# Performance work log

Hardware: AMD Instinct MI355X
Metric: run time of the kernel (lower is better)

## Reference

```python
import jax, jax.numpy as jnp
import numpy as np

B, J, D, H, W, AE, GH, NA, EH, L = 64, 20000, 32, 64, 4, 16, 24, 5000, 128, 32


def _ln(x, g=None, b=None, eps=1e-5):
    mu = x.mean(-1, keepdims=True)
    var = jnp.mean((x - mu) ** 2, axis=-1, keepdims=True)
    y = (x - mu) * jax.lax.rsqrt(var + eps)
    if g is not None:
        y = y * g + b
    return y


def setup_inputs():
    key = jax.random.key(0)
    ks = jax.random.split(key, 12)
    def rn(k, shape, s):
        return (jax.random.normal(k, shape) * s).astype(jnp.float32)
    return {
        "x": jax.random.normal(ks[0], (B, J), jnp.float32),
        "mask": jax.random.randint(ks[1], (B, J), 0, 2, jnp.int32),
        "atse_idx": jax.random.randint(ks[2], (J,), 0, NA, jnp.int32),
        "feature_embedding": jax.random.normal(ks[3], (J, D), jnp.float32),
        "atse_embedding": jax.random.normal(ks[4], (NA, AE), jnp.float32),
        "h_W1": rn(ks[5], (1 + D, H), 0.15), "h_b1": jnp.zeros((H,), jnp.float32),
        "h_ln1_g": jnp.ones((H,), jnp.float32), "h_ln1_b": jnp.zeros((H,), jnp.float32),
        "h_W2": rn(ks[6], (H, D), 0.12), "h_b2": jnp.zeros((D,), jnp.float32),
        "h_ln2_g": jnp.ones((D,), jnp.float32), "h_ln2_b": jnp.zeros((D,), jnp.float32),
        "g_W1": rn(ks[7], (D + AE, GH), 0.14), "g_b1": jnp.zeros((GH,), jnp.float32),
        "g_W2": rn(ks[8], (GH, W), 0.2), "g_b2": jnp.zeros((W,), jnp.float32),
        "c_W": rn(ks[9], (W * D, D), 0.09), "c_b": jnp.zeros((D,), jnp.float32),
        "c_ln_g": jnp.ones((D,), jnp.float32), "c_ln_b": jnp.zeros((D,), jnp.float32),
        "e_W1": rn(ks[10], (D, EH), 0.18), "e_b1": jnp.zeros((EH,), jnp.float32),
        "e_W2": rn(ks[11], (EH, 2 * L), 0.09), "e_b2": jnp.zeros((2 * L,), jnp.float32),
    }


def _forward(x, mask, atse_idx, feature_embedding, atse_embedding,
             h_W1, h_b1, h_ln1_g, h_ln1_b, h_W2, h_b2, h_ln2_g, h_ln2_b,
             g_W1, g_b1, g_W2, g_b2, c_W, c_b, c_ln_g, c_ln_b,
             e_W1, e_b1, e_W2, e_b2):
    TEMP = 1.0  # temperature_fixed=True -> scale = temperature_value
    Bv, Jv = x.shape
    Dv = feature_embedding.shape[1]
    # h-layer on all (b, j) pairs; LayerNorm/ReLU are per-row so this equals the
    # per-sample gather version on observed rows (unobserved rows get zero weight below).
    h_in = jnp.concatenate(
        [x[..., None], jnp.broadcast_to(feature_embedding[None], (Bv, Jv, Dv))], axis=-1)
    h = jax.nn.relu(_ln(h_in @ h_W1 + h_b1, h_ln1_g, h_ln1_b))
    h_out = jax.nn.relu(_ln(h @ h_W2 + h_b2, h_ln2_g, h_ln2_b))  # [B, J, D]
    # gate: [h_out | E_atse(j)] -> W head logits
    ae = atse_embedding[atse_idx]  # [J, AE]
    gate_in = jnp.concatenate(
        [h_out, jnp.broadcast_to(ae[None], (Bv, Jv, ae.shape[1]))], axis=-1)
    raw = jax.nn.relu(gate_in @ g_W1 + g_b1) @ g_W2 + g_b2  # [B, J, W]
    logits = jnp.clip(raw * TEMP, -10.0, 10.0)
    obs = mask.astype(bool)
    masked = jnp.where(obs[..., None], logits, -1e9)
    weights = jax.nn.softmax(masked, axis=1)  # softmax over observed junctions per head
    head_sums = jnp.einsum('bjw,bjd->bwd', weights, h_out)  # [B, W, D]
    Wn, Dn = head_sums.shape[1], head_sums.shape[2]
    combined = jax.nn.relu(_ln(head_sums.reshape(Bv, Wn * Dn) @ c_W + c_b, c_ln_g, c_ln_b))
    combined = jnp.where(obs.any(axis=1)[:, None], combined, 0.0)  # empty-mask rows -> zeros
    # encoder_mlp: scvi FCLayers, 2 layers, LayerNorm (no affine) + ReLU each
    e1 = jax.nn.relu(_ln(combined @ e_W1 + e_b1))
    mu_logvar = jax.nn.relu(_ln(e1 @ e_W2 + e_b2))
    mu, logvar = jnp.split(mu_logvar, 2, axis=-1)
    return mu, logvar


def reference(x, mask, atse_idx, feature_embedding, atse_embedding,
              h_W1, h_b1, h_ln1_g, h_ln1_b, h_W2, h_b2, h_ln2_g, h_ln2_b,
              g_W1, g_b1, g_W2, g_b2, c_W, c_b, c_ln_g, c_ln_b,
              e_W1, e_b1, e_W2, e_b2):
    return _forward(x, mask, atse_idx, feature_embedding, atse_embedding,
                    h_W1, h_b1, h_ln1_g, h_ln1_b, h_W2, h_b2, h_ln2_g, h_ln2_b,
                    g_W1, g_b1, g_W2, g_b2, c_W, c_b, c_ln_g, c_ln_b,
                    e_W1, e_b1, e_W2, e_b2)
```

## Files before the change

### kernel.cpp

```cpp
#include <hip/hip_runtime.h>
#include <hip/hip_bf16.h>
#include <math.h>

#define Bv 64
#define Jv 20000
#define NBT 8
#define NYB 125
#define ITERS 5

typedef __attribute__((ext_vector_type(8))) short short8;
typedef __attribute__((ext_vector_type(4))) float f32x4;
typedef __attribute__((ext_vector_type(2))) float f32x2;
typedef __attribute__((ext_vector_type(2))) unsigned int u32x2;

union U8 { short8 s; unsigned int u[4]; };

__device__ __forceinline__ unsigned short f2bf(float f) {
  unsigned int u = __float_as_uint(f);
  u += 0x7FFFu + ((u >> 16) & 1u);
  return (unsigned short)(u >> 16);
}
__device__ __forceinline__ unsigned int pkbf(float a, float b) {
  __hip_bfloat162 h = __float22bfloat162_rn(make_float2(a, b));
  union { __hip_bfloat162 h; unsigned int u; } c;
  c.h = h;
  return c.u;
}

__device__ __forceinline__ f32x2 pk_fma(f32x2 a, f32x2 b, f32x2 c) {
  return __builtin_elementwise_fma(a, b, c);
}
__device__ __forceinline__ f32x2 pk_max0(f32x2 a) {
  f32x2 z = {0.f, 0.f};
  return __builtin_elementwise_max(a, z);
}

template <int CTRL>
__device__ __forceinline__ float dppadd(float v) {
  int t = __builtin_amdgcn_update_dpp(0, __float_as_int(v), CTRL, 0xF, 0xF, true);
  return v + __int_as_float(t);
}
__device__ __forceinline__ float pl16sum(float v) {
  float a = v, b;
  asm("v_mov_b32 %1, %0\n\t"
      "v_permlane16_swap_b32 %0, %1"
      : "+v"(a), "=&v"(b));
  return a + b;
}
__device__ __forceinline__ float pl32sum(float v) {
  float a = v, b;
  asm("v_mov_b32 %1, %0\n\t"
      "v_permlane32_swap_b32 %0, %1"
      : "+v"(a), "=&v"(b));
  return a + b;
}

__global__ __launch_bounds__(256, 2) void pe_fused(
    const float* __restrict__ x, const int* __restrict__ mask,
    const int* __restrict__ atse_idx, const float* __restrict__ fe,
    const float* __restrict__ ae,
    const float* __restrict__ hW1, const float* __restrict__ hb1,
    const float* __restrict__ hl1g, const float* __restrict__ hl1b,
    const float* __restrict__ hW2, const float* __restrict__ hb2,
    const float* __restrict__ hl2g, const float* __restrict__ hl2b,
    const float* __restrict__ gW1, const float* __restrict__ gb1,
    const float* __restrict__ gW2, const float* __restrict__ gb2,
    float* __restrict__ acc_g, float* __restrict__ se_g) {
  __shared__ __align__(16) float s_pg[32 * 68];
  __shared__ __align__(16) float s_gb[32 * 24 + 16];
  __shared__ __align__(16) float s_pair[256 * 4];
  __shared__ __align__(16) float s_ae[32 * 20];
  __shared__ __align__(16) float s_w0[64], s_w0g[64], s_l1g[64], s_l1b[64];
  __shared__ __align__(16) float s_b2[32], s_l2g[32], s_l2b[32];
  __shared__ __align__(16) float s_gb1[24], s_gW2[96];
  __shared__ float s_gb2[4], s_scal[2];
  __shared__ __align__(16) float s_gW1aT[24 * 16];
  __shared__ unsigned char s_mk[256];
  __shared__ __align__(16) unsigned short s_ovl[256 * 36];

  int tid = threadIdx.x;
  int btile = blockIdx.x;
  int ytile = blockIdx.y;
  int lane = tid & 63, wv = tid >> 6;
  int li = lane & 15, quad = lane >> 4;
  unsigned short* s_h = s_ovl;
  unsigned short* s_gW1bf = (unsigned short*)s_pair;

  for (int i = tid; i < 768; i += 256) s_gW1bf[i] = f2bf(gW1[i]);
  for (int i = tid; i < 384; i += 256)
    s_gW1aT[i] = gW1[768 + (i & 15) * 24 + (i >> 4)];
  if (tid < 96) s_gW2[tid] = gW2[tid];
  if (tid < 64) { s_w0[tid] = hW1[tid]; s_l1g[tid] = hl1g[tid]; s_l1b[tid] = hl1b[tid]; }
  if (tid < 32) { s_b2[tid] = hb2[tid]; s_l2g[tid] = hl2g[tid]; s_l2b[tid] = hl2b[tid]; }
  if (tid < 24) s_gb1[tid] = gb1[tid];
  if (tid < 4) s_gb2[tid] = gb2[tid];
  if (tid >= 224 && tid < 240) s_gb[32 * 24 + (tid - 224)] = 0.f;

  short8 bW2[2][2];
#pragma unroll
  for (int kt = 0; kt < 2; ++kt)
#pragma unroll
    for (int nt = 0; nt < 2; ++nt) {
      U8 t;
#pragma unroll
      for (int p = 0; p < 4; ++p) {
        float lo = hW2[(kt * 32 + quad * 8 + 2 * p) * 32 + nt * 16 + li];
        float hi = hW2[(kt * 32 + quad * 8 + 2 * p + 1) * 32 + nt * 16 + li];
        t.u[p] = pkbf(lo, hi);
      }
      bW2[kt][nt] = t.s;
    }
  U8 bH;
#pragma unroll
  for (int p = 0; p < 4; ++p) {
    float lo = hW1[(1 + quad * 8 + 2 * p) * 64 + wv * 16 + li];
    float hi = hW1[(1 + quad * 8 + 2 * p + 1) * 64 + wv * 16 + li];
    bH.u[p] = pkbf(lo, hi);
  }
  float hb = hb1[wv * 16 + li];

  __syncthreads();
  if (tid < 64) s_w0g[tid] = s_w0[tid] * s_l1g[tid];
  if (tid == 64) {
    float sw = 0.f, qw = 0.f;
    for (int k = 0; k < 64; ++k) { float w = s_w0[k]; sw += w; qw = fmaf(w, w, qw); }
    s_scal[0] = sw; s_scal[1] = qw;
  }
  short8 aG0, aG1;
#pragma unroll
  for (int i = 0; i < 8; ++i) {
    int k = quad * 8 + i;
    aG0[i] = (short)s_gW1bf[k * 24 + li];
    aG1[i] = (li < 8) ? (short)s_gW1bf[k * 24 + 16 + li] : (short)0;
  }

  f32x4 racc[2][2];
#pragma unroll
  for (int a = 0; a < 2; ++a)
#pragma unroll
    for (int c = 0; c < 2; ++c) {
      racc[a][c][0] = 0.f; racc[a][c][1] = 0.f; racc[a][c][2] = 0.f; racc[a][c][3] = 0.f;
    }
  float seacc[2] = {0.f, 0.f};

  int jp8 = tid >> 3, b8 = tid & 7;
  int J0 = ytile * ITERS * 32;
  float xv; int mk;

  {
    if (tid < 128) {
      int jj = tid >> 2, q = tid & 3;
      int ai = atse_idx[J0 + jj];
      float4 av = *(const float4*)(ae + (size_t)ai * 16 + q * 4);
      *(float4*)(s_ae + jj * 20 + q * 4) = av;
    }
    size_t xo = (size_t)(btile * 8 + b8) * Jv + J0 + jp8;
    xv = x[xo];
    mk = mask[xo];
    f32x4 cP;
#pragma unroll
    for (int mt = 0; mt < 2; ++mt) {
      cP[0] = hb; cP[1] = hb; cP[2] = hb; cP[3] = hb;
      const float* fp = fe + (size_t)(J0 + mt * 16 + li) * 32 + quad * 8;
      float4 f0 = *(const float4*)fp;
      float4 f1 = *(const float4*)(fp + 4);
      U8 aF;
      aF.u[0] = pkbf(f0.x, f0.y); aF.u[1] = pkbf(f0.z, f0.w);
      aF.u[2] = pkbf(f1.x, f1.y); aF.u[3] = pkbf(f1.z, f1.w);
      cP = __builtin_amdgcn_mfma_f32_16x16x32_bf16(aF.s, bH.s, cP, 0, 0, 0);
#pragma unroll
      for (int r = 0; r < 4; ++r)
        s_pg[(mt * 16 + quad * 4 + r) * 68 + wv * 16 + li] = cP[r];
    }
  }
  __syncthreads();

  for (int it = 0; it < ITERS; ++it) {
    {
      int c0 = b8 * 3;
      const f32x2* ar2 = (const f32x2*)(s_ae + jp8 * 20);
      f32x2 A[8];
#pragma unroll
      for (int a = 0; a < 8; ++a) A[a] = ar2[a];
#pragma unroll
      for (int c = 0; c < 3; ++c) {
        const f32x2* tr2 = (const f32x2*)(s_gW1aT + (c0 + c) * 16);
        f32x2 g2 = {s_gb1[c0 + c], 0.f};
#pragma unroll
        for (int a = 0; a < 8; ++a) g2 = pk_fma(A[a], tr2[a], g2);
        s_gb[jp8 * 24 + c0 + c] = g2.x + g2.y;
      }
    }
    {
      const f32x2* pp2 = (const f32x2*)(s_pg + jp8 * 68 + b8 * 8);
      const f32x2* ww2 = (const f32x2*)(s_w0 + b8 * 8);
      f32x2 p2[4] = {pp2[0], pp2[1], pp2[2], pp2[3]};
      f32x2 s2 = (p2[0] + p2[1]) + (p2[2] + p2[3]);
      f32x2 q2 = pk_fma(p2[0], p2[0],
                 pk_fma(p2[1], p2[1],
                 pk_fma(p2[2], p2[2], p2[3] * p2[3])));
      f32x2 d2 = pk_fma(p2[0], ww2[0],
                 pk_fma(p2[1], ww2[1],
                 pk_fma(p2[2], ww2[2], p2[3] * ww2[3])));
      float sp = s2.x + s2.y, qp = q2.x + q2.y, dwp = d2.x + d2.y;
      sp = dppadd<0xB1>(sp); sp = dppadd<0x4E>(sp); sp = dppadd<0x141>(sp);
      qp = dppadd<0xB1>(qp); qp = dppadd<0x4E>(qp); qp = dppadd<0x141>(qp);
      dwp = dppadd<0xB1>(dwp); dwp = dppadd<0x4E>(dwp); dwp = dppadd<0x141>(dwp);
      if (b8 == 0) *(float4*)(s_pg + jp8 * 68 + 64) = make_float4(sp, qp, dwp, 0.f);
    }
    {
      float4 exv = *(const float4*)(s_pg + jp8 * 68 + 64);
      float mu1 = fmaf(xv, s_scal[0], exv.x) * 0.015625f;
      float Et2 = fmaf(xv * xv, s_scal[1], fmaf(2.0f * xv, exv.z, exv.y)) * 0.015625f;
      float rs1 = rsqrtf(fmaxf(Et2 - mu1 * mu1, 0.f) + 1e-5f);
      *(float4*)(s_pair + tid * 4) = make_float4(xv * rs1, rs1, -mu1 * rs1, 0.f);
      s_mk[tid] = (unsigned char)mk;
    }

    {
      f32x4 cd[4][2];
      float b2a = s_b2[li], b2b = s_b2[16 + li];
#pragma unroll
      for (int t = 0; t < 4; ++t) {
        cd[t][0][0] = b2a; cd[t][0][1] = b2a; cd[t][0][2] = b2a; cd[t][0][3] = b2a;
        cd[t][1][0] = b2b; cd[t][1][1] = b2b; cd[t][1][2] = b2b; cd[t][1][3] = b2b;
      }
#pragma unroll
      for (int kt = 0; kt < 2; ++kt) {
        int base = kt * 32 + quad * 8;
        float4 wg0 = *(const float4*)(s_w0g + base);
        float4 wg1 = *(const float4*)(s_w0g + base + 4);
        float4 gg0 = *(const float4*)(s_l1g + base);
        float4 gg1 = *(const float4*)(s_l1g + base + 4);
        float4 bb0 = *(const float4*)(s_l1b + base);
        float4 bb1 = *(const float4*)(s_l1b + base + 4);
        f32x2 wg2[4] = {{wg0.x, wg0.y}, {wg0.z, wg0.w}, {wg1.x, wg1.y}, {wg1.z, wg1.w}};
        f32x2 gg2[4] = {{gg0.x, gg0.y}, {gg0.z, gg0.w}, {gg1.x, gg1.y}, {gg1.z, gg1.w}};
        f32x2 bb2[4] = {{bb0.x, bb0.y}, {bb0.z, bb0.w}, {bb1.x, bb1.y}, {bb1.z, bb1.w}};
#pragma unroll
        for (int t = 0; t < 4; ++t) {
          int mrow = wv * 64 + t * 16 + li;
          float4 pr = *(const float4*)(s_pair + mrow * 4);
          f32x2 prx = {pr.x, pr.x}, pry = {pr.y, pr.y}, prz = {pr.z, pr.z};
          const float* pgp = s_pg + (mrow >> 3) * 68 + base;
          float4 p0 = *(const float4*)pgp;
          float4 p1 = *(const float4*)(pgp + 4);
          f32x2 pv2[4] = {{p0.x, p0.y}, {p0.z, p0.w}, {p1.x, p1.y}, {p1.z, p1.w}};
          U8 a8;
#pragma unroll
          for (int i = 0; i < 4; ++i) {
            f32x2 av2 = pk_max0(pk_fma(pk_fma(pry, pv2[i], prz), gg2[i],
                                       pk_fma(prx, wg2[i], bb2[i])));
            a8.u[i] = pkbf(av2.x, av2.y);
          }
          cd[t][0] = __builtin_amdgcn_mfma_f32_16x16x32_bf16(a8.s, bW2[kt][0], cd[t][0], 0, 0, 0);
          cd[t][1] = __builtin_amdgcn_mfma_f32_16x16x32_bf16(a8.s, bW2[kt][1], cd[t][1], 0, 0, 0);
        }
      }
      float g0 = s_l2g[li], be0 = s_l2b[li];
      float g1v = s_l2g[16 + li], be1 = s_l2b[16 + li];
#pragma unroll
      for (int t = 0; t < 4; ++t) {
        float sum[4], sq[4];
#pragma unroll
        for (int r = 0; r < 4; ++r) {
          float a = cd[t][0][r], b = cd[t][1][r];
          sum[r] = a + b;
          sq[r] = fmaf(a, a, b * b);
        }
#pragma unroll
        for (int r = 0; r < 4; ++r) {
          sum[r] = dppadd<0xB1>(sum[r]); sum[r] = dppadd<0x4E>(sum[r]);
          sum[r] = dppadd<0x124>(sum[r]); sum[r] = dppadd<0x128>(sum[r]);
          sq[r] = dppadd<0xB1>(sq[r]); sq[r] = dppadd<0x4E>(sq[r]);
          sq[r] = dppadd<0x124>(sq[r]); sq[r] = dppadd<0x128>(sq[r]);
        }
#pragma unroll
        for (int r = 0; r < 4; ++r) {
          float mu = sum[r] * 0.03125f;
          float var = sq[r] * 0.03125f - mu * mu;
          float rs2 = rsqrtf(fmaxf(var, 0.f) + 1e-5f);
          int m = wv * 64 + t * 16 + quad * 4 + r;
          float h0 = fmaxf(fmaf((cd[t][0][r] - mu) * rs2, g0, be0), 0.f);
          float h1 = fmaxf(fmaf((cd[t][1][r] - mu) * rs2, g1v, be1), 0.f);
          s_h[m * 36 + li] = f2bf(h0);
          s_h[m * 36 + 16 + li] = f2bf(h1);
        }
      }
    }

    {
      float4 gw4[2][4];
#pragma unroll
      for (int mt = 0; mt < 2; ++mt)
#pragma unroll
        for (int r = 0; r < 4; ++r) {
          int c = mt * 16 + quad * 4 + r;
          gw4[mt][r] = (c < 24) ? ((const float4*)s_gW2)[c]
                                : make_float4(0.f, 0.f, 0.f, 0.f);
        }
#pragma unroll
      for (int nt = 0; nt < 4; ++nt) {
        int m = wv * 64 + nt * 16 + li;
        U8 bu;
        const u32x2* hp2 = (const u32x2*)(s_h + m * 36 + quad * 8);
        u32x2 h01 = hp2[0], h23 = hp2[1];
        bu.u[0] = h01[0]; bu.u[1] = h01[1]; bu.u[2] = h23[0]; bu.u[3] = h23[1];
        int j = m >> 3;
        float4 cc0 = *(const float4*)(s_gb + j * 24 + quad * 4);
        float4 cc1 = *(const float4*)(s_gb + j * 24 + 16 + quad * 4);
        f32x4 c0, c1;
        c0[0] = cc0.x; c0[1] = cc0.y; c0[2] = cc0.z; c0[3] = cc0.w;
        c1[0] = cc1.x; c1[1] = cc1.y; c1[2] = cc1.z; c1[3] = cc1.w;
        c0 = __builtin_amdgcn_mfma_f32_16x16x32_bf16(aG0, bu.s, c0, 0, 0, 0);
        c1 = __builtin_amdgcn_mfma_f32_16x16x32_bf16(aG1, bu.s, c1, 0, 0, 0);
        f32x2 r01 = {s_gb2[0], s_gb2[1]};
        f32x2 r23 = {s_gb2[2], s_gb2[3]};
#pragma unroll
        for (int r = 0; r < 4; ++r) {
          float v0 = fmaxf(c0[r], 0.f);
          float v1 = fmaxf(c1[r], 0.f);
          f32x2 v0b = {v0, v0}, v1b = {v1, v1};
          float4 ga = gw4[0][r], gb = gw4[1][r];
          f32x2 ga01 = {ga.x, ga.y}, ga23 = {ga.z, ga.w};
          f32x2 gb01 = {gb.x, gb.y}, gb23 = {gb.z, gb.w};
          r01 = pk_fma(v0b, ga01, pk_fma(v1b, gb01, r01));
          r23 = pk_fma(v0b, ga23, pk_fma(v1b, gb23, r23));
        }
        float r0 = pl32sum(pl16sum(r01.x));
        float r1 = pl32sum(pl16sum(r01.y));
        float r2 = pl32sum(pl16sum(r23.x));
        float r3 = pl32sum(pl16sum(r23.y));
        r0 = fminf(fmaxf(r0, -10.f), 10.f);
        r1 = fminf(fmaxf(r1, -10.f), 10.f);
        r2 = fminf(fmaxf(r2, -10.f), 10.f);
        r3 = fminf(fmaxf(r3, -10.f), 10.f);
        bool act = (s_mk[m] != 0);
        float e0 = act ? __expf(r0 - 10.f) : 0.f;
        float e1 = act ? __expf(r1 - 10.f) : 0.f;
        float e2 = act ? __expf(r2 - 10.f) : 0.f;
        float e3 = act ? __expf(r3 - 10.f) : 0.f;
        if (quad == 0) *(float4*)(s_pair + m * 4) = make_float4(e0, e1, e2, e3);
      }
    }
    __syncthreads();

    bool has_next = (it + 1 < ITERS);
    int J0n = J0 + 32;
    float4 nf0, nf1, nf2, nf3, nav;
    float nxv = 0.f; int nmk = 0;
    if (has_next) {
      if (tid < 128) {
        int jj = tid >> 2, q = tid & 3;
        int ai = atse_idx[J0n + jj];
        nav = *(const float4*)(ae + (size_t)ai * 16 + q * 4);
      }
      const float* fp0 = fe + (size_t)(J0n + li) * 32 + quad * 8;
      const float* fp1 = fe + (size_t)(J0n + 16 + li) * 32 + quad * 8;
      nf0 = *(const float4*)fp0; nf1 = *(const float4*)(fp0 + 4);
      nf2 = *(const float4*)fp1; nf3 = *(const float4*)(fp1 + 4);
      size_t xo = (size_t)(btile * 8 + b8) * Jv + J0n + jp8;
      nxv = x[xo];
      nmk = mask[xo];
    }
    {
      const float* s_e2 = s_pair;
#pragma unroll
      for (int bs = 0; bs < 2; ++bs) {
        int b = wv * 2 + bs;
        float ev[8];
        float sep = 0.f;
#pragma unroll
        for (int i = 0; i < 8; ++i) {
          float v = s_e2[((quad * 8 + i) * 8 + b) * 4 + (li & 3)];
          v = (li < 4) ? v : 0.f;
          ev[i] = v;
          sep += v;
        }
        seacc[bs] += sep;
        U8 a8;
        a8.u[0] = pkbf(ev[0], ev[1]); a8.u[1] = pkbf(ev[2], ev[3]);
        a8.u[2] = pkbf(ev[4], ev[5]); a8.u[3] = pkbf(ev[6], ev[7]);
#pragma unroll
        for (int half = 0; half < 2; ++half) {
          U8 bh;
#pragma unroll
          for (int p = 0; p < 4; ++p) {
            unsigned int lo = s_h[((quad * 8 + 2 * p) * 8 + b) * 36 + half * 16 + li];
            unsigned int hi = s_h[((quad * 8 + 2 * p + 1) * 8 + b) * 36 + half * 16 + li];
            bh.u[p] = lo | (hi << 16);
          }
          racc[bs][half] = __builtin_amdgcn_mfma_f32_16x16x32_bf16(a8.s, bh.s, racc[bs][half], 0, 0, 0);
        }
      }
    }
    if (has_next) {
      if (tid < 128) {
        int jj = tid >> 2, q = tid & 3;
        *(float4*)(s_ae + jj * 20 + q * 4) = nav;
      }
      f32x4 cP;
#pragma unroll
      for (int mt = 0; mt < 2; ++mt) {
        cP[0] = hb; cP[1] = hb; cP[2] = hb; cP[3] = hb;
        U8 aF;
        if (mt == 0) {
          aF.u[0] = pkbf(nf0.x, nf0.y); aF.u[1] = pkbf(nf0.z, nf0.w);
          aF.u[2] = pkbf(nf1.x, nf1.y); aF.u[3] = pkbf(nf1.z, nf1.w);
        } else {
          aF.u[0] = pkbf(nf2.x, nf2.y); aF.u[1] = pkbf(nf2.z, nf2.w);
          aF.u[2] = pkbf(nf3.x, nf3.y); aF.u[3] = pkbf(nf3.z, nf3.w);
        }
        cP = __builtin_amdgcn_mfma_f32_16x16x32_bf16(aF.s, bH.s, cP, 0, 0, 0);
#pragma unroll
        for (int r = 0; r < 4; ++r)
          s_pg[(mt * 16 + quad * 4 + r) * 68 + wv * 16 + li] = cP[r];
      }
      xv = nxv; mk = nmk;
      J0 = J0n;
      __syncthreads();
    }
  }

#pragma unroll
  for (int bs = 0; bs < 2; ++bs) {
    float se = seacc[bs];
    se = pl32sum(pl16sum(se));
    if (quad == 0) {
      int bg = btile * 8 + wv * 2 + bs;
      float* dst = acc_g + (size_t)bg * 128;
#pragma unroll
      for (int half = 0; half < 2; ++half)
#pragma unroll
        for (int r = 0; r < 4; ++r)
          atomicAdd(dst + r * 32 + half * 16 + li, racc[bs][half][r]);
      if (li < 4) atomicAdd(&se_g[bg * 4 + li], se);
    }
  }
}

__global__ __launch_bounds__(256) void pe_tail(
    const float* __restrict__ acc_g, const float* __restrict__ se_g,
    const float* __restrict__ cW, const float* __restrict__ cb,
    const float* __restrict__ clng, const float* __restrict__ clnb,
    const float* __restrict__ eW1, const float* __restrict__ eb1,
    const float* __restrict__ eW2, const float* __restrict__ eb2,
    float* __restrict__ out) {
  int b = blockIdx.x;
  int tid = threadIdx.x;
  __shared__ float s_hs[128], s_cp[32], s_comb[32], s_e1[128], s_o2[64];
  __shared__ float s_red[4];

  float se0 = se_g[b * 4 + 0];
  bool empty = !(se0 > 0.0f);
  if (tid < 128) {
    float sw = se_g[b * 4 + (tid >> 5)];
    float inv = empty ? 0.0f : 1.0f / sw;
    s_hs[tid] = acc_g[b * 128 + tid] * inv;
  }
  __syncthreads();

  {
    int o = tid >> 3, seg = tid & 7;
    float p = 0.f;
#pragma unroll
    for (int i = 0; i < 16; ++i) {
      int k = seg * 16 + i;
      p = fmaf(s_hs[k], cW[k * 32 + o], p);
    }
    p += __shfl_xor(p, 1);
    p += __shfl_xor(p, 2);
    p += __shfl_xor(p, 4);
    if (seg == 0) s_cp[o] = p + cb[o];
  }
  __syncthreads();

  if (tid < 32) {
    float cp = s_cp[tid];
    float ssum = cp;
#pragma unroll
    for (int off = 16; off > 0; off >>= 1) ssum += __shfl_xor(ssum, off, 32);
    float mu = ssum * (1.0f / 32.0f);
    float dd = cp - mu;
    float sq = dd * dd;
#pragma unroll
    for (int off = 16; off > 0; off >>= 1) sq += __shfl_xor(sq, off, 32);
    float rs = rsqrtf(sq * (1.0f / 32.0f) + 1e-5f);
    float comb = fmaxf(fmaf(dd * rs, clng[tid], clnb[tid]), 0.0f);
    if (empty) comb = 0.0f;
    s_comb[tid] = comb;
  }
  __syncthreads();

  float v1 = 0.f;
  if (tid < 128) {
    v1 = eb1[tid];
#pragma unroll
    for (int i = 0; i < 32; ++i) v1 = fmaf(s_comb[i], eW1[i * 128 + tid], v1);
    float ss = v1, sq = v1 * v1;
#pragma unroll
    for (int off = 32; off > 0; off >>= 1) {
      ss += __shfl_xor(ss, off);
      sq += __shfl_xor(sq, off);
    }
    if ((tid & 63) == 0) {
      s_red[(tid >> 6) * 2] = ss;
      s_red[(tid >> 6) * 2 + 1] = sq;
    }
  }
  __syncthreads();
  if (tid < 128) {
    float ssT = s_red[0] + s_red[2];
    float sqT = s_red[1] + s_red[3];
    float mu = ssT * (1.0f / 128.0f);
    float var = sqT * (1.0f / 128.0f) - mu * mu;
    float rs = rsqrtf(fmaxf(var, 0.f) + 1e-5f);
    s_e1[tid] = fmaxf((v1 - mu) * rs, 0.0f);
  }
  __syncthreads();

  {
    int o = tid >> 2, sg = tid & 3;
    float v = 0.f;
#pragma unroll
    for (int i = 0; i < 32; ++i) {
      int k = sg * 32 + i;
      v = fmaf(s_e1[k], eW2[k * 64 + o], v);
    }
    v += __shfl_xor(v, 1);
    v += __shfl_xor(v, 2);
    if (sg == 0) s_o2[o] = v + eb2[o];
  }
  __syncthreads();

  if (tid < 64) {
    float v = s_o2[tid];
    float ss = v, sq = v * v;
#pragma unroll
    for (int off = 32; off > 0; off >>= 1) {
      ss += __shfl_xor(ss, off);
      sq += __shfl_xor(sq, off);
    }
    float mu = ss * (1.0f / 64.0f);
    float var = sq * (1.0f / 64.0f) - mu * mu;
    float rs = rsqrtf(fmaxf(var, 0.f) + 1e-5f);
    float o = fmaxf((v - mu) * rs, 0.0f);
    if (tid < 32)
      out[b * 32 + tid] = o;
    else
      out[Bv * 32 + b * 32 + (tid - 32)] = o;
  }
}

extern "C" void kernel_launch(void* const* d_in, const int* in_sizes, int n_in,
                              void* d_out, int out_size, void* d_ws, size_t ws_size,
                              hipStream_t stream) {
  const float* x    = (const float*)d_in[0];
  const int* mask   = (const int*)d_in[1];
  const int* atse   = (const int*)d_in[2];
  const float* fe   = (const float*)d_in[3];
  const float* ae   = (const float*)d_in[4];
  const float* hW1  = (const float*)d_in[5];
  const float* hb1  = (const float*)d_in[6];
  const float* hl1g = (const float*)d_in[7];
  const float* hl1b = (const float*)d_in[8];
  const float* hW2  = (const float*)d_in[9];
  const float* hb2  = (const float*)d_in[10];
  const float* hl2g = (const float*)d_in[11];
  const float* hl2b = (const float*)d_in[12];
  const float* gW1  = (const float*)d_in[13];
  const float* gb1  = (const float*)d_in[14];
  const float* gW2  = (const float*)d_in[15];
  const float* gb2  = (const float*)d_in[16];
  const float* cW   = (const float*)d_in[17];
  const float* cb   = (const float*)d_in[18];
  const float* clng = (const float*)d_in[19];
  const float* clnb = (const float*)d_in[20];
  const float* eW1  = (const float*)d_in[21];
  const float* eb1  = (const float*)d_in[22];
  const float* eW2  = (const float*)d_in[23];
  const float* eb2  = (const float*)d_in[24];
  float* out = (float*)d_out;

  float* ws = (float*)d_ws;
  float* accg = ws;
  float* seg  = accg + Bv * 128;

  hipMemsetAsync(accg, 0, (Bv * 128 + Bv * 4) * sizeof(float), stream);

  pe_fused<<<dim3(NBT, NYB), dim3(256), 0, stream>>>(
      x, mask, atse, fe, ae, hW1, hb1, hl1g, hl1b, hW2, hb2, hl2g, hl2b,
      gW1, gb1, gW2, gb2, accg, seg);
  pe_tail<<<dim3(Bv), dim3(256), 0, stream>>>(
      accg, seg, cW, cb, clng, clnb, eW1, eb1, eW2, eb2, out);
}
```

Before: 201.4 us.

## Retile fused kernel to loop over batch chunks per junction tile

Each block now handles one 32-junction tile across 32 batch rows in four 8-row chunks, instead of 8 batch rows across five junction tiles. The per-junction feature-embedding projection and gate bias are computed once per tile and reused for every batch chunk, which removes the prefetch and recompute of next-tile embeddings. The trade-off is that register accumulation is gone: every chunk issues its partial sums to global memory with atomics, so atomic traffic and contention grow substantially. The grid shape changes to 2x625 blocks and the occupancy hint of two blocks per multiprocessor is dropped from the launch bounds.

```diff
diff --git a/kernel.cpp b/kernel.cpp
--- a/kernel.cpp
+++ b/kernel.cpp
@@ -4,9 +4,9 @@
 
 #define Bv 64
 #define Jv 20000
-#define NBT 8
-#define NYB 125
-#define ITERS 5
+#define NBT 2
+#define NYB 625
+#define NCHUNK 4
 
 typedef __attribute__((ext_vector_type(8))) short short8;
 typedef __attribute__((ext_vector_type(4))) float f32x4;
@@ -55,7 +55,7 @@
   return a + b;
 }
 
-__global__ __launch_bounds__(256, 2) void pe_fused(
+__global__ __launch_bounds__(256) void pe_fused(
     const float* __restrict__ x, const int* __restrict__ mask,
     const int* __restrict__ atse_idx, const float* __restrict__ fe,
     const float* __restrict__ ae,
@@ -134,17 +134,8 @@
     aG1[i] = (li < 8) ? (short)s_gW1bf[k * 24 + 16 + li] : (short)0;
   }
 
-  f32x4 racc[2][2];
-#pragma unroll
-  for (int a = 0; a < 2; ++a)
-#pragma unroll
-    for (int c = 0; c < 2; ++c) {
-      racc[a][c][0] = 0.f; racc[a][c][1] = 0.f; racc[a][c][2] = 0.f; racc[a][c][3] = 0.f;
-    }
-  float seacc[2] = {0.f, 0.f};
-
   int jp8 = tid >> 3, b8 = tid & 7;
-  int J0 = ytile * ITERS * 32;
+  int J0 = ytile * 32;
   float xv; int mk;
 
   {
@@ -154,7 +145,7 @@
       float4 av = *(const float4*)(ae + (size_t)ai * 16 + q * 4);
       *(float4*)(s_ae + jj * 20 + q * 4) = av;
     }
-    size_t xo = (size_t)(btile * 8 + b8) * Jv + J0 + jp8;
+    size_t xo = (size_t)(btile * 32 + b8) * Jv + J0 + jp8;
     xv = x[xo];
     mk = mask[xo];
     f32x4 cP;
@@ -175,39 +166,40 @@
   }
   __syncthreads();
 
-  for (int it = 0; it < ITERS; ++it) {
-    {
-      int c0 = b8 * 3;
-      const f32x2* ar2 = (const f32x2*)(s_ae + jp8 * 20);
-      f32x2 A[8];
-#pragma unroll
-      for (int a = 0; a < 8; ++a) A[a] = ar2[a];
-#pragma unroll
-      for (int c = 0; c < 3; ++c) {
-        const f32x2* tr2 = (const f32x2*)(s_gW1aT + (c0 + c) * 16);
-        f32x2 g2 = {s_gb1[c0 + c], 0.f};
-#pragma unroll
-        for (int a = 0; a < 8; ++a) g2 = pk_fma(A[a], tr2[a], g2);
-        s_gb[jp8 * 24 + c0 + c] = g2.x + g2.y;
-      }
-    }
-    {
-      const f32x2* pp2 = (const f32x2*)(s_pg + jp8 * 68 + b8 * 8);
-      const f32x2* ww2 = (const f32x2*)(s_w0 + b8 * 8);
-      f32x2 p2[4] = {pp2[0], pp2[1], pp2[2], pp2[3]};
-      f32x2 s2 = (p2[0] + p2[1]) + (p2[2] + p2[3]);
-      f32x2 q2 = pk_fma(p2[0], p2[0],
-                 pk_fma(p2[1], p2[1],
-                 pk_fma(p2[2], p2[2], p2[3] * p2[3])));
-      f32x2 d2 = pk_fma(p2[0], ww2[0],
-                 pk_fma(p2[1], ww2[1],
-                 pk_fma(p2[2], ww2[2], p2[3] * ww2[3])));
-      float sp = s2.x + s2.y, qp = q2.x + q2.y, dwp = d2.x + d2.y;
-      sp = dppadd<0xB1>(sp); sp = dppadd<0x4E>(sp); sp = dppadd<0x141>(sp);
-      qp = dppadd<0xB1>(qp); qp = dppadd<0x4E>(qp); qp = dppadd<0x141>(qp);
-      dwp = dppadd<0xB1>(dwp); dwp = dppadd<0x4E>(dwp); dwp = dppadd<0x141>(dwp);
-      if (b8 == 0) *(float4*)(s_pg + jp8 * 68 + 64) = make_float4(sp, qp, dwp, 0.f);
-    }
+  {
+    int c0 = b8 * 3;
+    const f32x2* ar2 = (const f32x2*)(s_ae + jp8 * 20);
+    f32x2 A[8];
+#pragma unroll
+    for (int a = 0; a < 8; ++a) A[a] = ar2[a];
+#pragma unroll
+    for (int c = 0; c < 3; ++c) {
+      const f32x2* tr2 = (const f32x2*)(s_gW1aT + (c0 + c) * 16);
+      f32x2 g2 = {s_gb1[c0 + c], 0.f};
+#pragma unroll
+      for (int a = 0; a < 8; ++a) g2 = pk_fma(A[a], tr2[a], g2);
+      s_gb[jp8 * 24 + c0 + c] = g2.x + g2.y;
+    }
+  }
+  {
+    const f32x2* pp2 = (const f32x2*)(s_pg + jp8 * 68 + b8 * 8);
+    const f32x2* ww2 = (const f32x2*)(s_w0 + b8 * 8);
+    f32x2 p2[4] = {pp2[0], pp2[1], pp2[2], pp2[3]};
+    f32x2 s2 = (p2[0] + p2[1]) + (p2[2] + p2[3]);
+    f32x2 q2 = pk_fma(p2[0], p2[0],
+               pk_fma(p2[1], p2[1],
+               pk_fma(p2[2], p2[2], p2[3] * p2[3])));
+    f32x2 d2 = pk_fma(p2[0], ww2[0],
+               pk_fma(p2[1], ww2[1],
+               pk_fma(p2[2], ww2[2], p2[3] * ww2[3])));
+    float sp = s2.x + s2.y, qp = q2.x + q2.y, dwp = d2.x + d2.y;
+    sp = dppadd<0xB1>(sp); sp = dppadd<0x4E>(sp); sp = dppadd<0x141>(sp);
+    qp = dppadd<0xB1>(qp); qp = dppadd<0x4E>(qp); qp = dppadd<0x141>(qp);
+    dwp = dppadd<0xB1>(dwp); dwp = dppadd<0x4E>(dwp); dwp = dppadd<0x141>(dwp);
+    if (b8 == 0) *(float4*)(s_pg + jp8 * 68 + 64) = make_float4(sp, qp, dwp, 0.f);
+  }
+
+  for (int ck = 0; ck < NCHUNK; ++ck) {
     {
       float4 exv = *(const float4*)(s_pg + jp8 * 68 + 64);
       float mu1 = fmaf(xv, s_scal[0], exv.x) * 0.015625f;
@@ -345,26 +337,16 @@
     }
     __syncthreads();
 
-    bool has_next = (it + 1 < ITERS);
-    int J0n = J0 + 32;
-    float4 nf0, nf1, nf2, nf3, nav;
+    bool has_next = (ck + 1 < NCHUNK);
     float nxv = 0.f; int nmk = 0;
     if (has_next) {
-      if (tid < 128) {
-        int jj = tid >> 2, q = tid & 3;
-        int ai = atse_idx[J0n + jj];
-        nav = *(const float4*)(ae + (size_t)ai * 16 + q * 4);
-      }
-      const float* fp0 = fe + (size_t)(J0n + li) * 32 + quad * 8;
-      const float* fp1 = fe + (size_t)(J0n + 16 + li) * 32 + quad * 8;
-      nf0 = *(const float4*)fp0; nf1 = *(const float4*)(fp0 + 4);
-      nf2 = *(const float4*)fp1; nf3 = *(const float4*)(fp1 + 4);
-      size_t xo = (size_t)(btile * 8 + b8) * Jv + J0n + jp8;
+      size_t xo = (size_t)(btile * 32 + (ck + 1) * 8 + b8) * Jv + J0 + jp8;
       nxv = x[xo];
       nmk = mask[xo];
     }
     {
       const float* s_e2 = s_pair;
+      int cb0 = btile * 32 + ck * 8;
 #pragma unroll
       for (int bs = 0; bs < 2; ++bs) {
         int b = wv * 2 + bs;
@@ -377,7 +359,7 @@
           ev[i] = v;
           sep += v;
         }
-        seacc[bs] += sep;
+        sep = pl32sum(pl16sum(sep));
         U8 a8;
         a8.u[0] = pkbf(ev[0], ev[1]); a8.u[1] = pkbf(ev[2], ev[3]);
         a8.u[2] = pkbf(ev[4], ev[5]); a8.u[3] = pkbf(ev[6], ev[7]);
@@ -390,51 +372,22 @@
             unsigned int hi = s_h[((quad * 8 + 2 * p + 1) * 8 + b) * 36 + half * 16 + li];
             bh.u[p] = lo | (hi << 16);
           }
-          racc[bs][half] = __builtin_amdgcn_mfma_f32_16x16x32_bf16(a8.s, bh.s, racc[bs][half], 0, 0, 0);
-        }
+          f32x4 c = {0.f, 0.f, 0.f, 0.f};
+          c = __builtin_amdgcn_mfma_f32_16x16x32_bf16(a8.s, bh.s, c, 0, 0, 0);
+          if (quad == 0) {
+            float* dst = acc_g + (size_t)(cb0 + b) * 128;
+#pragma unroll
+            for (int r = 0; r < 4; ++r)
+              atomicAdd(dst + r * 32 + half * 16 + li, c[r]);
+          }
+        }
+        if (quad == 0 && li < 4)
+          atomicAdd(&se_g[(cb0 + b) * 4 + li], sep);
       }
     }
     if (has_next) {
-      if (tid < 128) {
-        int jj = tid >> 2, q = tid & 3;
-        *(float4*)(s_ae + jj * 20 + q * 4) = nav;
-      }
-      f32x4 cP;
-#pragma unroll
-      for (int mt = 0; mt < 2; ++mt) {
-        cP[0] = hb; cP[1] = hb; cP[2] = hb; cP[3] = hb;
-        U8 aF;
-        if (mt == 0) {
-          aF.u[0] = pkbf(nf0.x, nf0.y); aF.u[1] = pkbf(nf0.z, nf0.w);
-          aF.u[2] = pkbf(nf1.x, nf1.y); aF.u[3] = pkbf(nf1.z, nf1.w);
-        } else {
-          aF.u[0] = pkbf(nf2.x, nf2.y); aF.u[1] = pkbf(nf2.z, nf2.w);
-          aF.u[2] = pkbf(nf3.x, nf3.y); aF.u[3] = pkbf(nf3.z, nf3.w);
-        }
-        cP = __builtin_amdgcn_mfma_f32_16x16x32_bf16(aF.s, bH.s, cP, 0, 0, 0);
-#pragma unroll
-        for (int r = 0; r < 4; ++r)
-          s_pg[(mt * 16 + quad * 4 + r) * 68 + wv * 16 + li] = cP[r];
-      }
       xv = nxv; mk = nmk;
-      J0 = J0n;
       __syncthreads();
-    }
-  }
-
-#pragma unroll
-  for (int bs = 0; bs < 2; ++bs) {
-    float se = seacc[bs];
-    se = pl32sum(pl16sum(se));
-    if (quad == 0) {
-      int bg = btile * 8 + wv * 2 + bs;
-      float* dst = acc_g + (size_t)bg * 128;
-#pragma unroll
-      for (int half = 0; half < 2; ++half)
-#pragma unroll
-        for (int r = 0; r < 4; ++r)
-          atomicAdd(dst + r * 32 + half * 16 + li, racc[bs][half][r]);
-      if (li < 4) atomicAdd(&se_g[bg * 4 + li], se);
     }
   }
 }
```

Result: slower. 227.9 us (+13.2%).

## Hoist per-junction gate bias and LN stats into a separate precompute kernel

Applied to the files above, without the earlier changes.

Adds a pe_pre kernel that computes, once per junction, the atse-embedding gate bias and the sum, sum-of-squares and weight-dot statistics of the projected feature embedding, and writes them to workspace. Previously every one of the 8 batch-tile blocks recomputed these for the same junctions. The main kernel now loads the precomputed values from global memory into shared memory instead. This removes redundant compute and the atse gather from the hot loop, at the cost of an extra kernel launch and a global write/read round trip of about 20000×28 floats.

```diff
diff --git a/kernel.cpp b/kernel.cpp
--- a/kernel.cpp
+++ b/kernel.cpp
@@ -55,61 +55,33 @@
   return a + b;
 }
 
-__global__ __launch_bounds__(256, 2) void pe_fused(
-    const float* __restrict__ x, const int* __restrict__ mask,
+__global__ __launch_bounds__(256) void pe_pre(
     const int* __restrict__ atse_idx, const float* __restrict__ fe,
     const float* __restrict__ ae,
     const float* __restrict__ hW1, const float* __restrict__ hb1,
-    const float* __restrict__ hl1g, const float* __restrict__ hl1b,
-    const float* __restrict__ hW2, const float* __restrict__ hb2,
-    const float* __restrict__ hl2g, const float* __restrict__ hl2b,
     const float* __restrict__ gW1, const float* __restrict__ gb1,
-    const float* __restrict__ gW2, const float* __restrict__ gb2,
-    float* __restrict__ acc_g, float* __restrict__ se_g) {
+    float* __restrict__ gb_g, float* __restrict__ ex_g) {
+  __shared__ __align__(16) float s_ae[32 * 20];
   __shared__ __align__(16) float s_pg[32 * 68];
-  __shared__ __align__(16) float s_gb[32 * 24 + 16];
-  __shared__ __align__(16) float s_pair[256 * 4];
-  __shared__ __align__(16) float s_ae[32 * 20];
-  __shared__ __align__(16) float s_w0[64], s_w0g[64], s_l1g[64], s_l1b[64];
-  __shared__ __align__(16) float s_b2[32], s_l2g[32], s_l2b[32];
-  __shared__ __align__(16) float s_gb1[24], s_gW2[96];
-  __shared__ float s_gb2[4], s_scal[2];
+  __shared__ __align__(16) float s_w0[64];
   __shared__ __align__(16) float s_gW1aT[24 * 16];
-  __shared__ unsigned char s_mk[256];
-  __shared__ __align__(16) unsigned short s_ovl[256 * 36];
+  __shared__ __align__(16) float s_gb1[24];
 
   int tid = threadIdx.x;
-  int btile = blockIdx.x;
-  int ytile = blockIdx.y;
+  int J0 = blockIdx.x * 32;
   int lane = tid & 63, wv = tid >> 6;
   int li = lane & 15, quad = lane >> 4;
-  unsigned short* s_h = s_ovl;
-  unsigned short* s_gW1bf = (unsigned short*)s_pair;
-
-  for (int i = tid; i < 768; i += 256) s_gW1bf[i] = f2bf(gW1[i]);
+
   for (int i = tid; i < 384; i += 256)
     s_gW1aT[i] = gW1[768 + (i & 15) * 24 + (i >> 4)];
-  if (tid < 96) s_gW2[tid] = gW2[tid];
-  if (tid < 64) { s_w0[tid] = hW1[tid]; s_l1g[tid] = hl1g[tid]; s_l1b[tid] = hl1b[tid]; }
-  if (tid < 32) { s_b2[tid] = hb2[tid]; s_l2g[tid] = hl2g[tid]; s_l2b[tid] = hl2b[tid]; }
+  if (tid < 64) s_w0[tid] = hW1[tid];
   if (tid < 24) s_gb1[tid] = gb1[tid];
-  if (tid < 4) s_gb2[tid] = gb2[tid];
-  if (tid >= 224 && tid < 240) s_gb[32 * 24 + (tid - 224)] = 0.f;
-
-  short8 bW2[2][2];
-#pragma unroll
-  for (int kt = 0; kt < 2; ++kt)
-#pragma unroll
-    for (int nt = 0; nt < 2; ++nt) {
-      U8 t;
-#pragma unroll
-      for (int p = 0; p < 4; ++p) {
-        float lo = hW2[(kt * 32 + quad * 8 + 2 * p) * 32 + nt * 16 + li];
-        float hi = hW2[(kt * 32 + quad * 8 + 2 * p + 1) * 32 + nt * 16 + li];
-        t.u[p] = pkbf(lo, hi);
-      }
-      bW2[kt][nt] = t.s;
-    }
+  if (tid < 32) {
+    int ai = atse_idx[J0 + tid];
+    const float4* av4 = (const float4*)(ae + (size_t)ai * 16);
+#pragma unroll
+    for (int q = 0; q < 4; ++q) *(float4*)(s_ae + tid * 20 + q * 4) = av4[q];
+  }
   U8 bH;
 #pragma unroll
   for (int p = 0; p < 4; ++p) {
@@ -118,45 +90,9 @@
     bH.u[p] = pkbf(lo, hi);
   }
   float hb = hb1[wv * 16 + li];
-
-  __syncthreads();
-  if (tid < 64) s_w0g[tid] = s_w0[tid] * s_l1g[tid];
-  if (tid == 64) {
-    float sw = 0.f, qw = 0.f;
-    for (int k = 0; k < 64; ++k) { float w = s_w0[k]; sw += w; qw = fmaf(w, w, qw); }
-    s_scal[0] = sw; s_scal[1] = qw;
-  }
-  short8 aG0, aG1;
-#pragma unroll
-  for (int i = 0; i < 8; ++i) {
-    int k = quad * 8 + i;
-    aG0[i] = (short)s_gW1bf[k * 24 + li];
-    aG1[i] = (li < 8) ? (short)s_gW1bf[k * 24 + 16 + li] : (short)0;
-  }
-
-  f32x4 racc[2][2];
-#pragma unroll
-  for (int a = 0; a < 2; ++a)
-#pragma unroll
-    for (int c = 0; c < 2; ++c) {
-      racc[a][c][0] = 0.f; racc[a][c][1] = 0.f; racc[a][c][2] = 0.f; racc[a][c][3] = 0.f;
-    }
-  float seacc[2] = {0.f, 0.f};
-
-  int jp8 = tid >> 3, b8 = tid & 7;
-  int J0 = ytile * ITERS * 32;
-  float xv; int mk;
+  __syncthreads();
 
   {
-    if (tid < 128) {
-      int jj = tid >> 2, q = tid & 3;
-      int ai = atse_idx[J0 + jj];
-      float4 av = *(const float4*)(ae + (size_t)ai * 16 + q * 4);
-      *(float4*)(s_ae + jj * 20 + q * 4) = av;
-    }
-    size_t xo = (size_t)(btile * 8 + b8) * Jv + J0 + jp8;
-    xv = x[xo];
-    mk = mask[xo];
     f32x4 cP;
 #pragma unroll
     for (int mt = 0; mt < 2; ++mt) {
@@ -175,39 +111,155 @@
   }
   __syncthreads();
 
+  int jp8 = tid >> 3, b8 = tid & 7;
+  {
+    int c0 = b8 * 3;
+    const f32x2* ar2 = (const f32x2*)(s_ae + jp8 * 20);
+    f32x2 A[8];
+#pragma unroll
+    for (int a = 0; a < 8; ++a) A[a] = ar2[a];
+#pragma unroll
+    for (int c = 0; c < 3; ++c) {
+      const f32x2* tr2 = (const f32x2*)(s_gW1aT + (c0 + c) * 16);
+      f32x2 g2 = {s_gb1[c0 + c], 0.f};
+#pragma unroll
+      for (int a = 0; a < 8; ++a) g2 = pk_fma(A[a], tr2[a], g2);
+      gb_g[(size_t)(J0 + jp8) * 24 + c0 + c] = g2.x + g2.y;
+    }
+  }
+  {
+    const f32x2* pp2 = (const f32x2*)(s_pg + jp8 * 68 + b8 * 8);
+    const f32x2* ww2 = (const f32x2*)(s_w0 + b8 * 8);
+    f32x2 p2[4] = {pp2[0], pp2[1], pp2[2], pp2[3]};
+    f32x2 s2 = (p2[0] + p2[1]) + (p2[2] + p2[3]);
+    f32x2 q2 = pk_fma(p2[0], p2[0],
+               pk_fma(p2[1], p2[1],
+               pk_fma(p2[2], p2[2], p2[3] * p2[3])));
+    f32x2 d2 = pk_fma(p2[0], ww2[0],
+               pk_fma(p2[1], ww2[1],
+               pk_fma(p2[2], ww2[2], p2[3] * ww2[3])));
+    float sp = s2.x + s2.y, qp = q2.x + q2.y, dwp = d2.x + d2.y;
+    sp = dppadd<0xB1>(sp); sp = dppadd<0x4E>(sp); sp = dppadd<0x141>(sp);
+    qp = dppadd<0xB1>(qp); qp = dppadd<0x4E>(qp); qp = dppadd<0x141>(qp);
+    dwp = dppadd<0xB1>(dwp); dwp = dppadd<0x4E>(dwp); dwp = dppadd<0x141>(dwp);
+    if (b8 == 0)
+      *(float4*)(ex_g + (size_t)(J0 + jp8) * 4) = make_float4(sp, qp, dwp, 0.f);
+  }
+}
+
+__global__ __launch_bounds__(256, 2) void pe_fused(
+    const float* __restrict__ x, const int* __restrict__ mask,
+    const float* __restrict__ fe,
+    const float* __restrict__ hW1, const float* __restrict__ hb1,
+    const float* __restrict__ hl1g, const float* __restrict__ hl1b,
+    const float* __restrict__ hW2, const float* __restrict__ hb2,
+    const float* __restrict__ hl2g, const float* __restrict__ hl2b,
+    const float* __restrict__ gW1,
+    const float* __restrict__ gW2, const float* __restrict__ gb2,
+    const float* __restrict__ gb_g, const float* __restrict__ ex_g,
+    float* __restrict__ acc_g, float* __restrict__ se_g) {
+  __shared__ __align__(16) float s_pg[32 * 68];
+  __shared__ __align__(16) float s_gb[32 * 24 + 16];
+  __shared__ __align__(16) float s_pair[256 * 4];
+  __shared__ __align__(16) float s_w0[64], s_w0g[64], s_l1g[64], s_l1b[64];
+  __shared__ __align__(16) float s_b2[32], s_l2g[32], s_l2b[32];
+  __shared__ __align__(16) float s_gW2[96];
+  __shared__ float s_gb2[4], s_scal[2];
+  __shared__ unsigned char s_mk[256];
+  __shared__ __align__(16) unsigned short s_ovl[256 * 36];
+
+  int tid = threadIdx.x;
+  int btile = blockIdx.x;
+  int ytile = blockIdx.y;
+  int lane = tid & 63, wv = tid >> 6;
+  int li = lane & 15, quad = lane >> 4;
+  unsigned short* s_h = s_ovl;
+  unsigned short* s_gW1bf = (unsigned short*)s_pair;
+
+  for (int i = tid; i < 768; i += 256) s_gW1bf[i] = f2bf(gW1[i]);
+  if (tid < 96) s_gW2[tid] = gW2[tid];
+  if (tid < 64) { s_w0[tid] = hW1[tid]; s_l1g[tid] = hl1g[tid]; s_l1b[tid] = hl1b[tid]; }
+  if (tid < 32) { s_b2[tid] = hb2[tid]; s_l2g[tid] = hl2g[tid]; s_l2b[tid] = hl2b[tid]; }
+  if (tid < 4) s_gb2[tid] = gb2[tid];
+  if (tid >= 224 && tid < 240) s_gb[32 * 24 + (tid - 224)] = 0.f;
+
+  short8 bW2[2][2];
+#pragma unroll
+  for (int kt = 0; kt < 2; ++kt)
+#pragma unroll
+    for (int nt = 0; nt < 2; ++nt) {
+      U8 t;
+#pragma unroll
+      for (int p = 0; p < 4; ++p) {
+        float lo = hW2[(kt * 32 + quad * 8 + 2 * p) * 32 + nt * 16 + li];
+        float hi = hW2[(kt * 32 + quad * 8 + 2 * p + 1) * 32 + nt * 16 + li];
+        t.u[p] = pkbf(lo, hi);
+      }
+      bW2[kt][nt] = t.s;
+    }
+  U8 bH;
+#pragma unroll
+  for (int p = 0; p < 4; ++p) {
+    float lo = hW1[(1 + quad * 8 + 2 * p) * 64 + wv * 16 + li];
+    float hi = hW1[(1 + quad * 8 + 2 * p + 1) * 64 + wv * 16 + li];
+    bH.u[p] = pkbf(lo, hi);
+  }
+  float hb = hb1[wv * 16 + li];
+
+  __syncthreads();
+  if (tid < 64) s_w0g[tid] = s_w0[tid] * s_l1g[tid];
+  if (tid == 64) {
+    float sw = 0.f, qw = 0.f;
+    for (int k = 0; k < 64; ++k) { float w = s_w0[k]; sw += w; qw = fmaf(w, w, qw); }
+    s_scal[0] = sw; s_scal[1] = qw;
+  }
+  short8 aG0, aG1;
+#pragma unroll
+  for (int i = 0; i < 8; ++i) {
+    int k = quad * 8 + i;
+    aG0[i] = (short)s_gW1bf[k * 24 + li];
+    aG1[i] = (li < 8) ? (short)s_gW1bf[k * 24 + 16 + li] : (short)0;
+  }
+
+  f32x4 racc[2][2];
+#pragma unroll
+  for (int a = 0; a < 2; ++a)
+#pragma unroll
+    for (int c = 0; c < 2; ++c) {
+      racc[a][c][0] = 0.f; racc[a][c][1] = 0.f; racc[a][c][2] = 0.f; racc[a][c][3] = 0.f;
+    }
+  float seacc[2] = {0.f, 0.f};
+
+  int jp8 = tid >> 3, b8 = tid & 7;
+  int J0 = ytile * ITERS * 32;
+  float xv; int mk;
+
+  {
+    for (int i = tid; i < 768; i += 256) s_gb[i] = gb_g[(size_t)J0 * 24 + i];
+    if (tid < 128)
+      s_pg[(tid >> 2) * 68 + 64 + (tid & 3)] = ex_g[(size_t)J0 * 4 + tid];
+    size_t xo = (size_t)(btile * 8 + b8) * Jv + J0 + jp8;
+    xv = x[xo];
+    mk = mask[xo];
+    f32x4 cP;
+#pragma unroll
+    for (int mt = 0; mt < 2; ++mt) {
+      cP[0] = hb; cP[1] = hb; cP[2] = hb; cP[3] = hb;
+      const float* fp = fe + (size_t)(J0 + mt * 16 + li) * 32 + quad * 8;
+      float4 f0 = *(const float4*)fp;
+      float4 f1 = *(const float4*)(fp + 4);
+      U8 aF;
+      aF.u[0] = pkbf(f0.x, f0.y); aF.u[1] = pkbf(f0.z, f0.w);
+      aF.u[2] = pkbf(f1.x, f1.y); aF.u[3] = pkbf(f1.z, f1.w);
+      cP = __builtin_amdgcn_mfma_f32_16x16x32_bf16(aF.s, bH.s, cP, 0, 0, 0);
+#pragma unroll
+      for (int r = 0; r < 4; ++r)
+        s_pg[(mt * 16 + quad * 4 + r) * 68 + wv * 16 + li] = cP[r];
+    }
+  }
+  __syncthreads();
+
   for (int it = 0; it < ITERS; ++it) {
-    {
-      int c0 = b8 * 3;
-      const f32x2* ar2 = (const f32x2*)(s_ae + jp8 * 20);
-      f32x2 A[8];
-#pragma unroll
-      for (int a = 0; a < 8; ++a) A[a] = ar2[a];
-#pragma unroll
-      for (int c = 0; c < 3; ++c) {
-        const f32x2* tr2 = (const f32x2*)(s_gW1aT + (c0 + c) * 16);
-        f32x2 g2 = {s_gb1[c0 + c], 0.f};
-#pragma unroll
-        for (int a = 0; a < 8; ++a) g2 = pk_fma(A[a], tr2[a], g2);
-        s_gb[jp8 * 24 + c0 + c] = g2.x + g2.y;
-      }
-    }
-    {
-      const f32x2* pp2 = (const f32x2*)(s_pg + jp8 * 68 + b8 * 8);
-      const f32x2* ww2 = (const f32x2*)(s_w0 + b8 * 8);
-      f32x2 p2[4] = {pp2[0], pp2[1], pp2[2], pp2[3]};
-      f32x2 s2 = (p2[0] + p2[1]) + (p2[2] + p2[3]);
-      f32x2 q2 = pk_fma(p2[0], p2[0],
-                 pk_fma(p2[1], p2[1],
-                 pk_fma(p2[2], p2[2], p2[3] * p2[3])));
-      f32x2 d2 = pk_fma(p2[0], ww2[0],
-                 pk_fma(p2[1], ww2[1],
-                 pk_fma(p2[2], ww2[2], p2[3] * ww2[3])));
-      float sp = s2.x + s2.y, qp = q2.x + q2.y, dwp = d2.x + d2.y;
-      sp = dppadd<0xB1>(sp); sp = dppadd<0x4E>(sp); sp = dppadd<0x141>(sp);
-      qp = dppadd<0xB1>(qp); qp = dppadd<0x4E>(qp); qp = dppadd<0x141>(qp);
-      dwp = dppadd<0xB1>(dwp); dwp = dppadd<0x4E>(dwp); dwp = dppadd<0x141>(dwp);
-      if (b8 == 0) *(float4*)(s_pg + jp8 * 68 + 64) = make_float4(sp, qp, dwp, 0.f);
-    }
     {
       float4 exv = *(const float4*)(s_pg + jp8 * 68 + 64);
       float mu1 = fmaf(xv, s_scal[0], exv.x) * 0.015625f;
@@ -347,14 +399,12 @@
 
     bool has_next = (it + 1 < ITERS);
     int J0n = J0 + 32;
-    float4 nf0, nf1, nf2, nf3, nav;
+    float4 nf0, nf1, nf2, nf3;
     float nxv = 0.f; int nmk = 0;
     if (has_next) {
-      if (tid < 128) {
-        int jj = tid >> 2, q = tid & 3;
-        int ai = atse_idx[J0n + jj];
-        nav = *(const float4*)(ae + (size_t)ai * 16 + q * 4);
-      }
+      for (int i = tid; i < 768; i += 256) s_gb[i] = gb_g[(size_t)J0n * 24 + i];
+      if (tid < 128)
+        s_pg[(tid >> 2) * 68 + 64 + (tid & 3)] = ex_g[(size_t)J0n * 4 + tid];
       const float* fp0 = fe + (size_t)(J0n + li) * 32 + quad * 8;
       const float* fp1 = fe + (size_t)(J0n + 16 + li) * 32 + quad * 8;
       nf0 = *(const float4*)fp0; nf1 = *(const float4*)(fp0 + 4);
@@ -395,10 +445,6 @@
       }
     }
     if (has_next) {
-      if (tid < 128) {
-        int jj = tid >> 2, q = tid & 3;
-        *(float4*)(s_ae + jj * 20 + q * 4) = nav;
-      }
       f32x4 cP;
 #pragma unroll
       for (int mt = 0; mt < 2; ++mt) {
@@ -585,12 +631,16 @@
   float* ws = (float*)d_ws;
   float* accg = ws;
   float* seg  = accg + Bv * 128;
+  float* gbg  = seg + Bv * 4;
+  float* exg  = gbg + Jv * 24;
 
   hipMemsetAsync(accg, 0, (Bv * 128 + Bv * 4) * sizeof(float), stream);
 
+  pe_pre<<<dim3(625), dim3(256), 0, stream>>>(
+      atse, fe, ae, hW1, hb1, gW1, gb1, gbg, exg);
   pe_fused<<<dim3(NBT, NYB), dim3(256), 0, stream>>>(
-      x, mask, atse, fe, ae, hW1, hb1, hl1g, hl1b, hW2, hb2, hl2g, hl2b,
-      gW1, gb1, gW2, gb2, accg, seg);
+      x, mask, fe, hW1, hb1, hl1g, hl1b, hW2, hb2, hl2g, hl2b,
+      gW1, gW2, gb2, gbg, exg, accg, seg);
   pe_tail<<<dim3(Bv), dim3(256), 0, stream>>>(
       accg, seg, cW, cb, clng, clnb, eW1, eb1, eW2, eb2, out);
 }
```

New measurement: 205.5 us. +2.1%, slower.
